# Performance work log

Hardware: AMD Instinct MI355X
Metric: run time of the kernel (lower is better)

The kernel has to match this reference:

```python
import jax, jax.numpy as jnp
import numpy as np

B, N, C0, N0 = 2, 4096, 128, 10242
IN_CH = 19  # 16 class-label + 3 xyz channels of `original`
EPS = 1e-5


def setup_inputs() -> dict:
    key = jax.random.key(0)
    ks = jax.random.split(key, 8)
    original = jax.random.normal(ks[0], (B, IN_CH, N), dtype=jnp.float32)
    projected = jax.random.normal(ks[1], (B, C0, N0), dtype=jnp.float32)
    vertex = jax.random.normal(ks[2], (N0, 3), dtype=jnp.float32)
    near_idx = jax.random.randint(ks[3], (N0, 6), 1, N0)  # low=1 so threshold > 0
    W0 = jax.random.normal(ks[4], (128, IN_CH + C0), dtype=jnp.float32) * 0.02
    W1 = jax.random.normal(ks[5], (128, 128), dtype=jnp.float32) * 0.02
    W2 = jax.random.normal(ks[6], (128, 128), dtype=jnp.float32) * 0.02
    z = jnp.zeros((128,), jnp.float32)
    o = jnp.ones((128,), jnp.float32)
    return {
        'original': original, 'projected': projected, 'vertex': vertex,
        'near_idx': near_idx,
        'W0': W0, 'b0': z, 'g0': o, 'be0': z,
        'W1': W1, 'b1': z, 'g1': o, 'be1': z,
        'W2': W2, 'b2': z, 'g2': o, 'be2': z,
    }


def _sf_to_pc(proj_f, vertex, near_idx, xyz):
    # proj_f: [B, N0, C0] features per mesh vertex; xyz: [B, N, 3]
    r = jnp.sqrt(jnp.sum(vertex[0] ** 2))  # sphere radius of fractal mesh
    # spherical projection of xyz onto sphere radius r (same direction)
    pxyz = xyz * (r / jnp.linalg.norm(xyz, axis=-1, keepdims=True))  # [B,N,3]
    # threshold = dist(vertex[0], vertex[near_idx[0,0]]); compare squared dists
    t2 = jnp.sum((vertex[0] - vertex[near_idx[0, 0]]) ** 2)
    # squared distances via GEMM: |p|^2 = r^2 (on sphere)
    v2 = jnp.sum(vertex ** 2, axis=-1)  # [N0]
    d2 = r * r + v2[None, None, :] - 2.0 * jnp.einsum('bnd,md->bnm', pxyz, vertex)
    mask = d2 <= t2                              # [B,N,N0]
    has = jnp.any(mask, axis=-1)                 # [B,N]
    first = jnp.argmax(mask, axis=-1)            # first matching vertex (early-exit semantics)
    feat = jnp.take_along_axis(proj_f, first[..., None], axis=1)  # [B,N,C0]
    return jnp.where(has[..., None], feat, 0.0)


def _conv_bn_relu(x, W, b, g, be):
    # x: [B,N,Cin]; 1x1 Conv1d == per-point linear; BN over (B,N) per channel (train mode)
    y = jnp.einsum('bnc,oc->bno', x, W) + b
    mean = jnp.mean(y, axis=(0, 1))
    var = jnp.var(y, axis=(0, 1))
    y = g * (y - mean) * jax.lax.rsqrt(var + EPS) + be
    return jax.nn.relu(y)


def reference(original, projected, vertex, near_idx,
              W0, b0, g0, be0, W1, b1, g1, be1, W2, b2, g2, be2):
    orig = jnp.transpose(original, (0, 2, 1))    # [B,N,19]
    proj_f = jnp.transpose(projected, (0, 2, 1))  # [B,N0,C0]
    xyz = orig[:, :, :3]
    feat = _sf_to_pc(proj_f, vertex, near_idx, xyz)      # [B,N,C0]
    x = jnp.concatenate([orig, feat], axis=-1)           # [B,N,19+C0]
    x = _conv_bn_relu(x, W0, b0, g0, be0)
    x = _conv_bn_relu(x, W1, b1, g1, be1)
    x = _conv_bn_relu(x, W2, b2, g2, be2)
    return jnp.transpose(x, (0, 2, 1))  # [B,128,N]
```

## Files before the change

kernel.cpp:

```cpp
#include <hip/hip_runtime.h>

#define NPTS 4096
#define N0V  10242
#define EPSV 1e-5f
#define SLOTS 16

typedef unsigned short ushortT;
typedef __attribute__((ext_vector_type(8))) short short8;
typedef __attribute__((ext_vector_type(4))) float f32x4;

__device__ __forceinline__ float fmul(float a,float b){return __fmul_rn(a,b);}
__device__ __forceinline__ float fadd(float a,float b){return __fadd_rn(a,b);}
__device__ __forceinline__ float fsub(float a,float b){return __fsub_rn(a,b);}

__device__ __forceinline__ ushortT f2bf(float x){
  unsigned u = __float_as_uint(x);
  u = (u + 0x7fffu + ((u>>16)&1u)) >> 16;
  return (ushortT)u;
}
__device__ __forceinline__ float bf2f(ushortT u){
  return __uint_as_float(((unsigned)u) << 16);
}

template<int NS>
__device__ __forceinline__ void tile_mm(const ushortT* xa, const ushortT* wt, int wstr,
    int li, int hi, int rt, int colg, f32x4& acc)
{
  acc = (f32x4){0.f,0.f,0.f,0.f};
  const ushortT* wbp = wt + colg*wstr + hi*8;
  const ushortT* xap = xa + (rt*16 + li)*168 + hi*8;
  #pragma unroll
  for (int s=0;s<NS;s++){
    short8 bb = *(const short8*)(wbp + s*32);
    short8 a0 = *(const short8*)(xap + s*32);
    acc = __builtin_amdgcn_mfma_f32_16x16x32_bf16(a0, bb, acc, 0,0,0);
  }
}

__device__ __forceinline__ void tile_partials(const f32x4& acc, float* __restrict__ slotL,
                                              int blk, int lane, int colg)
{
  float s1=0.f, s2=0.f;
  #pragma unroll
  for (int r=0;r<4;r++){ s1 += acc[r]; s2 = fmaf(acc[r],acc[r],s2); }
  s1 += __shfl_xor(s1,16); s1 += __shfl_xor(s1,32);
  s2 += __shfl_xor(s2,16); s2 += __shfl_xor(s2,32);
  if (lane < 16){
    float* sl = slotL + (blk & (SLOTS-1))*256;
    atomicAdd(&sl[colg], s1);
    atomicAdd(&sl[128 + colg], s2);
  }
}

__device__ __forceinline__ void slot_stats(const float* __restrict__ slotL,
    const float* __restrict__ g, const float* __restrict__ be,
    float* red2, float* stS, float* stB, int t)
{
  if (t < 256){
    float v = 0.f;
    #pragma unroll
    for (int s=0;s<SLOTS;s++) v += slotL[s*256 + t];
    red2[t] = v;
  }
  __syncthreads();
  if (t < 128){
    float S = red2[t], Q = red2[128 + t];
    float mean = S * (1.0f/8192.0f);
    float var  = Q * (1.0f/8192.0f) - mean*mean;
    float inv  = 1.0f / __fsqrt_rn(var + EPSV);
    float sc = g[t]*inv;
    stS[t] = sc;
    stB[t] = be[t] - mean*sc;
  }
  __syncthreads();
}

__device__ __forceinline__ void dma_w(const ushortT* __restrict__ src, ushortT* dst,
                                      int nchunks, int w, int lane)
{
  const char* s = (const char*)src;
  char* d = (char*)dst;
  for (int i = w; i < nchunks; i += 16){
    __builtin_amdgcn_global_load_lds(
        (const __attribute__((address_space(1))) void*)(s + (size_t)i*1024 + (size_t)lane*16),
        (__attribute__((address_space(3))) void*)(d + (size_t)i*1024), 16, 0, 0);
  }
}

__global__ __launch_bounds__(1024) void k_l0(
    const float* __restrict__ orig, const float* __restrict__ proj,
    const float* __restrict__ vertex, const int* __restrict__ nidx,
    const float* __restrict__ W0, const float* __restrict__ b0,
    const float* __restrict__ W1, const float* __restrict__ W2,
    float* __restrict__ slot0, float* __restrict__ slotZ,
    ushortT* __restrict__ wpkg, ushortT* __restrict__ y0)
{
  __shared__ __align__(16) ushortT wt[128*168];
  __shared__ __align__(16) ushortT xa[32*168];

  const int t    = threadIdx.x;
  const int blk  = blockIdx.x;
  const int lane = t & 63;
  const int w    = t >> 6;
  const int b    = blk >> 7;
  const int n0   = (blk & 127) * 32;
  const int li   = lane & 15;
  const int hi   = lane >> 4;
  const int rt   = w >> 3;
  const int colg = (w & 7)*16 + li;

  if (blk < 8) slotZ[blk*1024 + t] = 0.f;

  if (t < 136){
    int u = blk*136 + t;
    int L = u / 17408, q = u - L*17408;
    int o = q / 136, k = q - o*136;
    float v = 0.f;
    if (k < 128) v = (L == 0) ? W1[o*128 + k] : W2[o*128 + k];
    wpkg[u] = f2bf(v);
  }

  for (int u = t; u < 21504; u += 1024){
    int o = u/168, k = u - o*168;
    wt[u] = f2bf((k < 147) ? W0[o*147 + k] : 0.f);
  }

  {
    float v0x=vertex[0], v0y=vertex[1], v0z=vertex[2];
    float r  = __fsqrt_rn(fadd(fadd(fmul(v0x,v0x),fmul(v0y,v0y)),fmul(v0z,v0z)));
    float rr = fmul(r,r);
    int j0 = nidx[0];
    float ax=vertex[3*j0], ay=vertex[3*j0+1], az=vertex[3*j0+2];
    float dx=fsub(v0x,ax), dy=fsub(v0y,ay), dz=fsub(v0z,az);
    float t2 = fadd(fadd(fmul(dx,dx),fmul(dy,dy)),fmul(dz,dz));

    #pragma unroll
    for (int rr_i=0; rr_i<2; rr_i++){
      const int row = w*2 + rr_i;
      const int n = n0 + row;
      const float* ob = orig + (b*19)*NPTS + n;
      float x=ob[0], y=ob[NPTS], z=ob[2*NPTS];
      float nrm = __fsqrt_rn(fadd(fadd(fmul(x,x),fmul(y,y)),fmul(z,z)));
      float s = __fdiv_rn(r,nrm);
      float px=fmul(x,s), py=fmul(y,s), pz=fmul(z,s);

      int first=0, has=0;
      for (int c0=0; c0<N0V; c0+=256){
        int m0=min(c0+lane,N0V-1), m1=min(c0+lane+64,N0V-1),
            m2=min(c0+lane+128,N0V-1), m3=min(c0+lane+192,N0V-1);
        float a0x=vertex[3*m0],a0y=vertex[3*m0+1],a0z=vertex[3*m0+2];
        float a1x=vertex[3*m1],a1y=vertex[3*m1+1],a1z=vertex[3*m1+2];
        float a2x=vertex[3*m2],a2y=vertex[3*m2+1],a2z=vertex[3*m2+2];
        float a3x=vertex[3*m3],a3y=vertex[3*m3+1],a3z=vertex[3*m3+2];
        float v20=fadd(fadd(fmul(a0x,a0x),fmul(a0y,a0y)),fmul(a0z,a0z));
        float v21=fadd(fadd(fmul(a1x,a1x),fmul(a1y,a1y)),fmul(a1z,a1z));
        float v22=fadd(fadd(fmul(a2x,a2x),fmul(a2y,a2y)),fmul(a2z,a2z));
        float v23=fadd(fadd(fmul(a3x,a3x),fmul(a3y,a3y)),fmul(a3z,a3z));
        float d0=fadd(fadd(fmul(px,a0x),fmul(py,a0y)),fmul(pz,a0z));
        float d1=fadd(fadd(fmul(px,a1x),fmul(py,a1y)),fmul(pz,a1z));
        float d2=fadd(fadd(fmul(px,a2x),fmul(py,a2y)),fmul(pz,a2z));
        float d3=fadd(fadd(fmul(px,a3x),fmul(py,a3y)),fmul(pz,a3z));
        bool h0 = (c0+lane    <N0V) && (fsub(fadd(rr,v20),fmul(2.0f,d0)) <= t2);
        bool h1 = (c0+lane+64 <N0V) && (fsub(fadd(rr,v21),fmul(2.0f,d1)) <= t2);
        bool h2 = (c0+lane+128<N0V) && (fsub(fadd(rr,v22),fmul(2.0f,d2)) <= t2);
        bool h3 = (c0+lane+192<N0V) && (fsub(fadd(rr,v23),fmul(2.0f,d3)) <= t2);
        unsigned long long bal;
        if ((bal=__ballot(h0))){ first=c0     +__builtin_ctzll(bal); has=1; break; }
        if ((bal=__ballot(h1))){ first=c0+ 64+__builtin_ctzll(bal); has=1; break; }
        if ((bal=__ballot(h2))){ first=c0+128+__builtin_ctzll(bal); has=1; break; }
        if ((bal=__ballot(h3))){ first=c0+192+__builtin_ctzll(bal); has=1; break; }
      }

      ushortT* rowp = xa + row*168;
      const float* pb = proj + (long)b*128*N0V;
      #pragma unroll
      for (int k=0;k<3;k++){
        int idx = lane + k*64;
        if (idx < 168){
          float v;
          if (idx < 19)        v = orig[(b*19+idx)*NPTS + n];
          else if (idx < 147)  v = has ? pb[(long)(idx-19)*N0V + first] : 0.0f;
          else                 v = 0.0f;
          rowp[idx] = f2bf(v);
        }
      }
    }
  }
  __syncthreads();

  f32x4 acc;
  tile_mm<5>(xa, wt, 168, li, hi, rt, colg, acc);
  float bo = b0[colg];
  #pragma unroll
  for (int r=0;r<4;r++) acc[r] += bo;
  tile_partials(acc, slot0, blk, lane, colg);
  #pragma unroll
  for (int r=0;r<4;r++)
    y0[(long)(b*4096 + n0 + rt*16 + hi*4 + r)*128 + colg] = f2bf(acc[r]);
}

__global__ __launch_bounds__(1024) void k_lmid(
    const ushortT* __restrict__ yin, const float* __restrict__ slotPrev,
    const float* __restrict__ g, const float* __restrict__ be,
    const ushortT* __restrict__ wpk, const float* __restrict__ bias,
    float* __restrict__ slotCur, ushortT* __restrict__ yout)
{
  __shared__ __align__(16) ushortT wt[128*136];
  __shared__ __align__(16) ushortT xa[32*168];
  __shared__ float red2[256];
  __shared__ float stS[128];
  __shared__ float stB[128];

  const int t    = threadIdx.x;
  const int blk  = blockIdx.x;
  const int lane = t & 63;
  const int w    = t >> 6;
  const int n0   = blk * 32;
  const int li   = lane & 15;
  const int hi   = lane >> 4;
  const int rt   = w >> 3;
  const int colg = (w & 7)*16 + li;

  dma_w(wpk, wt, 34, w, lane);

  for (int u = t; u < 1280; u += 1024){
    int row = u/40, c = 128 + (u - row*40);
    xa[row*168 + c] = 0;
  }
  slot_stats(slotPrev, g, be, red2, stS, stB, t);

  if (t < 512){
    int row = t >> 4, c0 = (t & 15) * 8;
    short8 yv = *(const short8*)(yin + (long)(n0+row)*128 + c0);
    short8 xv;
    #pragma unroll
    for (int j=0;j<8;j++){
      float f = bf2f((ushortT)yv[j]);
      f = fmaxf(fmaf(f, stS[c0+j], stB[c0+j]), 0.f);
      xv[j] = (short)f2bf(f);
    }
    *(short8*)(xa + row*168 + c0) = xv;
  }
  __syncthreads();

  f32x4 acc;
  tile_mm<4>(xa, wt, 136, li, hi, rt, colg, acc);
  float bo = bias[colg];
  #pragma unroll
  for (int r=0;r<4;r++) acc[r] += bo;
  tile_partials(acc, slotCur, blk, lane, colg);
  #pragma unroll
  for (int r=0;r<4;r++)
    yout[(long)(n0 + rt*16 + hi*4 + r)*128 + colg] = f2bf(acc[r]);
}

__global__ __launch_bounds__(1024) void k_out(
    const ushortT* __restrict__ yin, const float* __restrict__ slotPrev,
    const float* __restrict__ g, const float* __restrict__ be,
    float* __restrict__ out)
{
  __shared__ float ft[32*132];
  __shared__ float red2[256];
  __shared__ float stS[128];
  __shared__ float stB[128];

  const int t   = threadIdx.x;
  const int blk = blockIdx.x;
  const int b   = blk >> 7;
  const int n0  = (blk & 127) * 32;

  slot_stats(slotPrev, g, be, red2, stS, stB, t);

  if (t < 512){
    int row = t >> 4, c0 = (t & 15) * 8;
    short8 yv = *(const short8*)(yin + (long)(b*4096 + n0 + row)*128 + c0);
    #pragma unroll
    for (int j=0;j<8;j++)
      ft[row*132 + c0 + j] = fmaxf(fmaf(bf2f((ushortT)yv[j]), stS[c0+j], stB[c0+j]), 0.f);
  }
  __syncthreads();

  float* ob = out + (long)b*128*NPTS + n0;
  {
    int oo = t >> 3, jj = (t & 7) * 4;
    float4 v;
    v.x = ft[(jj  )*132 + oo];
    v.y = ft[(jj+1)*132 + oo];
    v.z = ft[(jj+2)*132 + oo];
    v.w = ft[(jj+3)*132 + oo];
    *(float4*)(ob + (long)oo*NPTS + jj) = v;
  }
}

extern "C" void kernel_launch(void* const* d_in, const int* in_sizes, int n_in,
                              void* d_out, int out_size, void* d_ws, size_t ws_size,
                              hipStream_t stream)
{
  const float* orig   = (const float*)d_in[0];
  const float* proj   = (const float*)d_in[1];
  const float* vertex = (const float*)d_in[2];
  const int*   nidx   = (const int*)d_in[3];
  const float* W0 = (const float*)d_in[4];
  const float* b0 = (const float*)d_in[5];
  const float* g0 = (const float*)d_in[6];
  const float* be0= (const float*)d_in[7];
  const float* W1 = (const float*)d_in[8];
  const float* b1 = (const float*)d_in[9];
  const float* g1 = (const float*)d_in[10];
  const float* be1= (const float*)d_in[11];
  const float* W2 = (const float*)d_in[12];
  const float* b2 = (const float*)d_in[13];
  const float* g2 = (const float*)d_in[14];
  const float* be2= (const float*)d_in[15];
  float* out = (float*)d_out;

  float*   ws    = (float*)d_ws;
  float*   slot0 = ws;
  float*   slot1 = ws + 4096;
  float*   slot2 = ws + 8192;
  ushortT* wpkg  = (ushortT*)(ws + 12288);
  ushortT* yA    = (ushortT*)(ws + 29696);
  ushortT* yB    = yA + 8192*128;

  hipMemsetAsync(d_ws, 0, 4096*sizeof(float), stream);

  k_l0  <<<256, 1024, 0, stream>>>(orig, proj, vertex, nidx, W0, b0, W1, W2,
                                   slot0, slot1, wpkg, yA);
  k_lmid<<<256, 1024, 0, stream>>>(yA, slot0, g0, be0, wpkg,         b1, slot1, yB);
  k_lmid<<<256, 1024, 0, stream>>>(yB, slot1, g1, be1, wpkg + 17408, b2, slot2, yA);
  k_out <<<256, 1024, 0, stream>>>(yA, slot2, g2, be2, out);
}
```

Measured before the change: 30.83 us.

## Add prep kernel transposing inputs to bf16 and use fixed-point stat atomics

A new prep kernel transposes projected features into a point-major bf16 layout, transposes the original input, packs vertices as float4 with precomputed squared norms, prebuilds bf16 weight packages and zeroes the slots. This replaces the hipMemset. The layer-0 kernel then gathers contiguous rows, DMAs its weights into LDS and loads one vector per vertex in the search loop, instead of doing strided gathers and per-block weight conversion. BN statistic accumulation switches to 64-bit fixed-point atomics, which makes the sums deterministic but adds a kernel launch and a full pass over the projected tensor.

```diff
diff --git a/kernel.cpp b/kernel.cpp
--- a/kernel.cpp
+++ b/kernel.cpp
@@ -4,8 +4,10 @@
 #define N0V  10242
 #define EPSV 1e-5f
 #define SLOTS 16
+#define FXS 16777216.0
 
 typedef unsigned short ushortT;
+typedef unsigned long long ullT;
 typedef __attribute__((ext_vector_type(8))) short short8;
 typedef __attribute__((ext_vector_type(4))) float f32x4;
 
@@ -37,7 +39,7 @@
   }
 }
 
-__device__ __forceinline__ void tile_partials(const f32x4& acc, float* __restrict__ slotL,
+__device__ __forceinline__ void tile_partials(const f32x4& acc, ullT* __restrict__ slotL,
                                               int blk, int lane, int colg)
 {
   float s1=0.f, s2=0.f;
@@ -46,21 +48,23 @@
   s1 += __shfl_xor(s1,16); s1 += __shfl_xor(s1,32);
   s2 += __shfl_xor(s2,16); s2 += __shfl_xor(s2,32);
   if (lane < 16){
-    float* sl = slotL + (blk & (SLOTS-1))*256;
-    atomicAdd(&sl[colg], s1);
-    atomicAdd(&sl[128 + colg], s2);
-  }
-}
-
-__device__ __forceinline__ void slot_stats(const float* __restrict__ slotL,
+    ullT* sl = slotL + (blk & (SLOTS-1))*256;
+    long long q1 = __double2ll_rn((double)s1 * FXS);
+    long long q2 = __double2ll_rn((double)s2 * FXS);
+    atomicAdd(&sl[colg],       (ullT)q1);
+    atomicAdd(&sl[128 + colg], (ullT)q2);
+  }
+}
+
+__device__ __forceinline__ void slot_stats(const ullT* __restrict__ slotL,
     const float* __restrict__ g, const float* __restrict__ be,
     float* red2, float* stS, float* stB, int t)
 {
   if (t < 256){
-    float v = 0.f;
+    long long v = 0;
     #pragma unroll
-    for (int s=0;s<SLOTS;s++) v += slotL[s*256 + t];
-    red2[t] = v;
+    for (int s=0;s<SLOTS;s++) v += (long long)slotL[s*256 + t];
+    red2[t] = (float)((double)v * (1.0/FXS));
   }
   __syncthreads();
   if (t < 128){
@@ -87,13 +91,84 @@
   }
 }
 
+__global__ __launch_bounds__(1024) void k_prep(
+    const float* __restrict__ proj, const float* __restrict__ orig,
+    const float* __restrict__ vertex,
+    const float* __restrict__ W0, const float* __restrict__ W1, const float* __restrict__ W2,
+    ullT* __restrict__ slots, ushortT* __restrict__ wpkg0, ushortT* __restrict__ wpkg12,
+    float* __restrict__ vpk, float* __restrict__ origT, ushortT* __restrict__ projT)
+{
+  __shared__ __align__(16) char lsb[40960];
+  const int blk = blockIdx.x, t = threadIdx.x;
+
+  if (blk < 162){
+    ushortT (*tile)[132] = (ushortT(*)[132])lsb;
+    int pb = blk / 81, mt = blk - pb*81, m0 = mt*128;
+    {
+      int c = t >> 3, ms = (t & 7) * 16;
+      const float* src = proj + ((long)pb*128 + c)*N0V;
+      #pragma unroll
+      for (int j=0;j<16;j++){
+        int m = m0 + ms + j;
+        tile[c][ms+j] = f2bf((m < N0V) ? src[m] : 0.f);
+      }
+    }
+    __syncthreads();
+    {
+      int ml = t >> 3, cs = (t & 7) * 16;
+      int m = m0 + ml;
+      if (m < N0V){
+        ushortT* dst = projT + ((long)pb*N0V + m)*128 + cs;
+        #pragma unroll
+        for (int j=0;j<16;j++) dst[j] = tile[cs+j][ml];
+      }
+    }
+  } else if (blk < 178){
+    float (*tile)[516] = (float(*)[516])lsb;
+    int u = blk - 162, pb = u >> 3, nt = u & 7, n0 = nt*512;
+    for (int i = t; i < 19*512; i += 1024){
+      int c = i >> 9, nn = i & 511;
+      tile[c][nn] = orig[((long)pb*19 + c)*NPTS + n0 + nn];
+    }
+    __syncthreads();
+    for (int i = t; i < 512*20; i += 1024){
+      int nn = i / 20, c = i - nn*20;
+      origT[((long)pb*NPTS + n0 + nn)*20 + c] = (c < 19) ? tile[c][nn] : 0.f;
+    }
+  } else if (blk < 181){
+    int u0 = (blk-178)*4096 + t*4;
+    slots[u0] = 0; slots[u0+1] = 0; slots[u0+2] = 0; slots[u0+3] = 0;
+  } else if (blk < 192){
+    int m = (blk-181)*1024 + t;
+    if (m < N0V){
+      float x = vertex[3*m], y = vertex[3*m+1], z = vertex[3*m+2];
+      float v2 = fadd(fadd(fmul(x,x),fmul(y,y)),fmul(z,z));
+      ((float4*)vpk)[m] = make_float4(x,y,z,v2);
+    }
+  } else if (blk < 213){
+    int u = (blk-192)*1024 + t;
+    if (u < 21504){
+      int o = u/168, k = u - o*168;
+      wpkg0[u] = f2bf((k < 147) ? W0[o*147 + k] : 0.f);
+    }
+  } else {
+    int u = (blk-213)*1024 + t;
+    if (u < 34816){
+      int L = u / 17408, q = u - L*17408;
+      int o = q/136, k = q - o*136;
+      float v = 0.f;
+      if (k < 128) v = L ? W2[o*128 + k] : W1[o*128 + k];
+      wpkg12[u] = f2bf(v);
+    }
+  }
+}
+
 __global__ __launch_bounds__(1024) void k_l0(
-    const float* __restrict__ orig, const float* __restrict__ proj,
+    const float* __restrict__ origT, const ushortT* __restrict__ projT,
+    const float* __restrict__ vpk,
     const float* __restrict__ vertex, const int* __restrict__ nidx,
-    const float* __restrict__ W0, const float* __restrict__ b0,
-    const float* __restrict__ W1, const float* __restrict__ W2,
-    float* __restrict__ slot0, float* __restrict__ slotZ,
-    ushortT* __restrict__ wpkg, ushortT* __restrict__ y0)
+    const ushortT* __restrict__ wpkg0, const float* __restrict__ b0,
+    ullT* __restrict__ slot0, ushortT* __restrict__ y0)
 {
   __shared__ __align__(16) ushortT wt[128*168];
   __shared__ __align__(16) ushortT xa[32*168];
@@ -109,21 +184,7 @@
   const int rt   = w >> 3;
   const int colg = (w & 7)*16 + li;
 
-  if (blk < 8) slotZ[blk*1024 + t] = 0.f;
-
-  if (t < 136){
-    int u = blk*136 + t;
-    int L = u / 17408, q = u - L*17408;
-    int o = q / 136, k = q - o*136;
-    float v = 0.f;
-    if (k < 128) v = (L == 0) ? W1[o*128 + k] : W2[o*128 + k];
-    wpkg[u] = f2bf(v);
-  }
-
-  for (int u = t; u < 21504; u += 1024){
-    int o = u/168, k = u - o*168;
-    wt[u] = f2bf((k < 147) ? W0[o*147 + k] : 0.f);
-  }
+  dma_w(wpkg0, wt, 42, w, lane);
 
   {
     float v0x=vertex[0], v0y=vertex[1], v0z=vertex[2];
@@ -133,13 +194,14 @@
     float ax=vertex[3*j0], ay=vertex[3*j0+1], az=vertex[3*j0+2];
     float dx=fsub(v0x,ax), dy=fsub(v0y,ay), dz=fsub(v0z,az);
     float t2 = fadd(fadd(fmul(dx,dx),fmul(dy,dy)),fmul(dz,dz));
+    const float4* vp4 = (const float4*)vpk;
 
     #pragma unroll
     for (int rr_i=0; rr_i<2; rr_i++){
       const int row = w*2 + rr_i;
       const int n = n0 + row;
-      const float* ob = orig + (b*19)*NPTS + n;
-      float x=ob[0], y=ob[NPTS], z=ob[2*NPTS];
+      const float* rowO = origT + ((long)b*NPTS + n)*20;
+      float x=rowO[0], y=rowO[1], z=rowO[2];
       float nrm = __fsqrt_rn(fadd(fadd(fmul(x,x),fmul(y,y)),fmul(z,z)));
       float s = __fdiv_rn(r,nrm);
       float px=fmul(x,s), py=fmul(y,s), pz=fmul(z,s);
@@ -148,22 +210,18 @@
       for (int c0=0; c0<N0V; c0+=256){
         int m0=min(c0+lane,N0V-1), m1=min(c0+lane+64,N0V-1),
             m2=min(c0+lane+128,N0V-1), m3=min(c0+lane+192,N0V-1);
-        float a0x=vertex[3*m0],a0y=vertex[3*m0+1],a0z=vertex[3*m0+2];
-        float a1x=vertex[3*m1],a1y=vertex[3*m1+1],a1z=vertex[3*m1+2];
-        float a2x=vertex[3*m2],a2y=vertex[3*m2+1],a2z=vertex[3*m2+2];
-        float a3x=vertex[3*m3],a3y=vertex[3*m3+1],a3z=vertex[3*m3+2];
-        float v20=fadd(fadd(fmul(a0x,a0x),fmul(a0y,a0y)),fmul(a0z,a0z));
-        float v21=fadd(fadd(fmul(a1x,a1x),fmul(a1y,a1y)),fmul(a1z,a1z));
-        float v22=fadd(fadd(fmul(a2x,a2x),fmul(a2y,a2y)),fmul(a2z,a2z));
-        float v23=fadd(fadd(fmul(a3x,a3x),fmul(a3y,a3y)),fmul(a3z,a3z));
-        float d0=fadd(fadd(fmul(px,a0x),fmul(py,a0y)),fmul(pz,a0z));
-        float d1=fadd(fadd(fmul(px,a1x),fmul(py,a1y)),fmul(pz,a1z));
-        float d2=fadd(fadd(fmul(px,a2x),fmul(py,a2y)),fmul(pz,a2z));
-        float d3=fadd(fadd(fmul(px,a3x),fmul(py,a3y)),fmul(pz,a3z));
-        bool h0 = (c0+lane    <N0V) && (fsub(fadd(rr,v20),fmul(2.0f,d0)) <= t2);
-        bool h1 = (c0+lane+64 <N0V) && (fsub(fadd(rr,v21),fmul(2.0f,d1)) <= t2);
-        bool h2 = (c0+lane+128<N0V) && (fsub(fadd(rr,v22),fmul(2.0f,d2)) <= t2);
-        bool h3 = (c0+lane+192<N0V) && (fsub(fadd(rr,v23),fmul(2.0f,d3)) <= t2);
+        float4 va = vp4[m0];
+        float4 vb = vp4[m1];
+        float4 vc = vp4[m2];
+        float4 vd = vp4[m3];
+        float d0=fadd(fadd(fmul(px,va.x),fmul(py,va.y)),fmul(pz,va.z));
+        float d1=fadd(fadd(fmul(px,vb.x),fmul(py,vb.y)),fmul(pz,vb.z));
+        float d2=fadd(fadd(fmul(px,vc.x),fmul(py,vc.y)),fmul(pz,vc.z));
+        float d3=fadd(fadd(fmul(px,vd.x),fmul(py,vd.y)),fmul(pz,vd.z));
+        bool h0 = (c0+lane    <N0V) && (fsub(fadd(rr,va.w),fmul(2.0f,d0)) <= t2);
+        bool h1 = (c0+lane+64 <N0V) && (fsub(fadd(rr,vb.w),fmul(2.0f,d1)) <= t2);
+        bool h2 = (c0+lane+128<N0V) && (fsub(fadd(rr,vc.w),fmul(2.0f,d2)) <= t2);
+        bool h3 = (c0+lane+192<N0V) && (fsub(fadd(rr,vd.w),fmul(2.0f,d3)) <= t2);
         unsigned long long bal;
         if ((bal=__ballot(h0))){ first=c0     +__builtin_ctzll(bal); has=1; break; }
         if ((bal=__ballot(h1))){ first=c0+ 64+__builtin_ctzll(bal); has=1; break; }
@@ -172,16 +230,16 @@
       }
 
       ushortT* rowp = xa + row*168;
-      const float* pb = proj + (long)b*128*N0V;
+      const ushortT* pr = projT + ((long)b*N0V + first)*128;
       #pragma unroll
       for (int k=0;k<3;k++){
         int idx = lane + k*64;
         if (idx < 168){
-          float v;
-          if (idx < 19)        v = orig[(b*19+idx)*NPTS + n];
-          else if (idx < 147)  v = has ? pb[(long)(idx-19)*N0V + first] : 0.0f;
-          else                 v = 0.0f;
-          rowp[idx] = f2bf(v);
+          ushortT v;
+          if (idx < 19)        v = f2bf(rowO[idx]);
+          else if (idx < 147)  v = has ? pr[idx-19] : (ushortT)0;
+          else                 v = 0;
+          rowp[idx] = v;
         }
       }
     }
@@ -200,10 +258,10 @@
 }
 
 __global__ __launch_bounds__(1024) void k_lmid(
-    const ushortT* __restrict__ yin, const float* __restrict__ slotPrev,
+    const ushortT* __restrict__ yin, const ullT* __restrict__ slotPrev,
     const float* __restrict__ g, const float* __restrict__ be,
     const ushortT* __restrict__ wpk, const float* __restrict__ bias,
-    float* __restrict__ slotCur, ushortT* __restrict__ yout)
+    ullT* __restrict__ slotCur, ushortT* __restrict__ yout)
 {
   __shared__ __align__(16) ushortT wt[128*136];
   __shared__ __align__(16) ushortT xa[32*168];
@@ -255,7 +313,7 @@
 }
 
 __global__ __launch_bounds__(1024) void k_out(
-    const ushortT* __restrict__ yin, const float* __restrict__ slotPrev,
+    const ushortT* __restrict__ yin, const ullT* __restrict__ slotPrev,
     const float* __restrict__ g, const float* __restrict__ be,
     float* __restrict__ out)
 {
@@ -314,19 +372,23 @@
   const float* be2= (const float*)d_in[15];
   float* out = (float*)d_out;
 
-  float*   ws    = (float*)d_ws;
-  float*   slot0 = ws;
-  float*   slot1 = ws + 4096;
-  float*   slot2 = ws + 8192;
-  ushortT* wpkg  = (ushortT*)(ws + 12288);
-  ushortT* yA    = (ushortT*)(ws + 29696);
-  ushortT* yB    = yA + 8192*128;
-
-  hipMemsetAsync(d_ws, 0, 4096*sizeof(float), stream);
-
-  k_l0  <<<256, 1024, 0, stream>>>(orig, proj, vertex, nidx, W0, b0, W1, W2,
-                                   slot0, slot1, wpkg, yA);
-  k_lmid<<<256, 1024, 0, stream>>>(yA, slot0, g0, be0, wpkg,         b1, slot1, yB);
-  k_lmid<<<256, 1024, 0, stream>>>(yB, slot1, g1, be1, wpkg + 17408, b2, slot2, yA);
+  float*   ws     = (float*)d_ws;
+  ullT*    slots  = (ullT*)ws;
+  ullT*    slot0  = slots;
+  ullT*    slot1  = slots + 4096;
+  ullT*    slot2  = slots + 8192;
+  ushortT* wpkg0  = (ushortT*)(ws + 24576);
+  ushortT* wpkg12 = (ushortT*)(ws + 35328);
+  float*   vpk    = ws + 52736;
+  float*   origT  = ws + 93704;
+  ushortT* projT  = (ushortT*)(ws + 257544);
+  ushortT* yA     = (ushortT*)(ws + 1568520);
+  ushortT* yB     = yA + 8192*128;
+
+  k_prep<<<247, 1024, 0, stream>>>(proj, orig, vertex, W0, W1, W2,
+                                   slots, wpkg0, wpkg12, vpk, origT, projT);
+  k_l0  <<<256, 1024, 0, stream>>>(origT, projT, vpk, vertex, nidx, wpkg0, b0, slot0, yA);
+  k_lmid<<<256, 1024, 0, stream>>>(yA, slot0, g0, be0, wpkg12,         b1, slot1, yB);
+  k_lmid<<<256, 1024, 0, stream>>>(yB, slot1, g1, be1, wpkg12 + 17408, b2, slot2, yA);
   k_out <<<256, 1024, 0, stream>>>(yA, slot2, g2, be2, out);
 }
```

After: 35.26 us. +14.4%, slower.
